# Optimization experiments

Measured on AMD Instinct MI355X. Metric: run time of the kernel, lower is better.

Reference implementation:

```python
import jax, jax.numpy as jnp
import numpy as np

N_NODES = 50000
N_EDGES = 400000


def setup_inputs() -> dict:
    key = jax.random.key(0)
    ks = jax.random.split(key, 8)
    d_in, d_hid, d_out = 512, 512, 256
    feats = jax.random.normal(ks[0], (N_NODES, d_in), dtype=jnp.float32)
    src = jax.random.randint(ks[1], (N_EDGES,), 0, N_NODES, dtype=jnp.int32)
    dst = jax.random.randint(ks[2], (N_EDGES,), 0, N_NODES, dtype=jnp.int32)
    # Glorot-ish scaled weights so activations stay O(1)
    W0 = jax.random.normal(ks[3], (d_in, d_hid), dtype=jnp.float32) / np.sqrt(d_in)
    b0 = jnp.zeros((d_hid,), jnp.float32)
    W1 = jax.random.normal(ks[4], (d_hid, d_hid), dtype=jnp.float32) / np.sqrt(d_hid)
    b1 = jnp.zeros((d_hid,), jnp.float32)
    W2 = jax.random.normal(ks[5], (d_hid, d_out), dtype=jnp.float32) / np.sqrt(d_hid)
    b2 = jnp.zeros((d_out,), jnp.float32)
    return {"feats": feats, "src": src, "dst": dst,
            "W0": W0, "b0": b0, "W1": W1, "b1": b1, "W2": W2, "b2": b2}


def _sage_conv_gcn(h, src, dst, W, b, deg):
    # DGL SAGEConv aggregator_type='gcn':
    # h_neigh[v] = (sum_{u->v} h[u] + h[v]) / (in_deg(v) + 1); out = h_neigh @ W + b
    agg = jax.ops.segment_sum(h[src], dst, num_segments=h.shape[0])  # [N, d]
    h_neigh = (agg + h) / (deg[:, None] + 1.0)
    return h_neigh @ W + b


def reference(feats, src, dst, W0, b0, W1, b1, W2, b2):
    N = feats.shape[0]
    deg = jax.ops.segment_sum(jnp.ones((src.shape[0],), feats.dtype), dst,
                              num_segments=N)  # in-degree per node
    h = jax.nn.relu(_sage_conv_gcn(feats, src, dst, W0, b0, deg))  # dropout p=0, norm none
    h = jax.nn.relu(_sage_conv_gcn(h, src, dst, W1, b1, deg))
    h = _sage_conv_gcn(h, src, dst, W2, b2, deg)  # final layer: no activation
    return h
```

## Files before the change

### kernel.cpp

```cpp
#include <hip/hip_runtime.h>
#include <stdint.h>

#define N_NODES 50000
#define N_EDGES 400000
#define MPAD    50048
#define SCAN_B  49

typedef __bf16 bf16x8 __attribute__((ext_vector_type(8)));
typedef float  f32x4  __attribute__((ext_vector_type(4)));
typedef unsigned short ushort_t;
typedef unsigned int   uint_t;

__device__ __forceinline__ ushort_t f2b(float f){
    uint_t x = __float_as_uint(f);
    x += 0x7FFFu + ((x >> 16) & 1u);
    return (ushort_t)(x >> 16);
}
__device__ __forceinline__ float b2f(ushort_t h){
    return __uint_as_float(((uint_t)h) << 16);
}

__device__ __forceinline__ int xcd_swz(int orig, int nwg){
    int q = nwg >> 3, r = nwg & 7;
    int xcd = orig & 7, idx = orig >> 3;
    int base = (xcd < r) ? xcd * (q + 1) : r * (q + 1) + (xcd - r) * q;
    return base + idx;
}

__global__ void zero_two(int* a, int* b, int n){
    int i = blockIdx.x * blockDim.x + threadIdx.x;
    if (i < n){ a[i] = 0; b[i] = 0; }
}

__global__ void hist_kernel(const int* __restrict__ dst, int* __restrict__ deg, int E){
    int i = blockIdx.x * blockDim.x + threadIdx.x;
    if (i < E) atomicAdd(&deg[dst[i]], 1);
}

__global__ __launch_bounds__(1024) void blk_scan_kernel(
        const int* __restrict__ deg, int* __restrict__ offs,
        int* __restrict__ bsum, int n){
    __shared__ int buf[1024];
    const int t = threadIdx.x, b = blockIdx.x;
    const int i = b * 1024 + t;
    int v = (i < n) ? deg[i] : 0;
    buf[t] = v; __syncthreads();
    for (int off = 1; off < 1024; off <<= 1){
        int x = (t >= off) ? buf[t - off] : 0;
        __syncthreads();
        buf[t] += x;
        __syncthreads();
    }
    if (i < n) offs[i] = buf[t] - v;
    if (t == 1023) bsum[b] = buf[1023];
}

__global__ void bsum_scan_kernel(int* __restrict__ bsum, int nb){
    int t = threadIdx.x;
    int orig = (t < nb) ? bsum[t] : 0;
    int v = orig;
    #pragma unroll
    for (int off = 1; off < 64; off <<= 1){
        int x = __shfl_up(v, off, 64);
        if (t >= off) v += x;
    }
    if (t < nb) bsum[t] = v - orig;
}

__global__ __launch_bounds__(1024) void add_off_kernel(
        int* __restrict__ offs, const int* __restrict__ bsum, int n){
    int i = blockIdx.x * 1024 + threadIdx.x;
    if (i < n) offs[i] += bsum[blockIdx.x];
    if (i == 0) offs[n] = N_EDGES;
}

__global__ void fill_kernel(const int* __restrict__ src, const int* __restrict__ dst,
                            const int* __restrict__ offs, int* __restrict__ cursor,
                            int* __restrict__ nbr, int E){
    int i = blockIdx.x * blockDim.x + threadIdx.x;
    if (i < E){
        int d = dst[i];
        int p = atomicAdd(&cursor[d], 1);
        nbr[offs[d] + p] = src[i];
    }
}

__global__ __launch_bounds__(256) void wtrans3_kernel(
        const float* __restrict__ W0, const float* __restrict__ W1,
        const float* __restrict__ W2, ushort_t* __restrict__ W0t,
        ushort_t* __restrict__ W1t, ushort_t* __restrict__ W2t){
    __shared__ float t[32][33];
    int b = blockIdx.x;
    const float* W; ushort_t* Wt; int K, N, bx, by;
    if (b < 256){            W = W0; Wt = W0t; K = 512; N = 512;
                             bx = (b & 15) * 32; by = (b >> 4) * 32; }
    else if (b < 512){ b -= 256; W = W1; Wt = W1t; K = 512; N = 512;
                             bx = (b & 15) * 32; by = (b >> 4) * 32; }
    else {             b -= 512; W = W2; Wt = W2t; K = 512; N = 256;
                             bx = (b & 7) * 32;  by = (b >> 3) * 32; }
    const int x = threadIdx.x & 31, y = threadIdx.x >> 5;
    #pragma unroll
    for (int j = 0; j < 32; j += 8)
        t[y + j][x] = W[(size_t)(by + y + j) * N + bx + x];
    __syncthreads();
    #pragma unroll
    for (int j = 0; j < 32; j += 8)
        Wt[(size_t)(bx + y + j) * K + by + x] = f2b(t[x][y + j]);
}

__device__ __forceinline__ void load16(const void* g, void* l){
    __builtin_amdgcn_global_load_lds((const __attribute__((address_space(1))) void*)g,
                                     (__attribute__((address_space(3))) void*)l, 16, 0, 0);
}

__global__ __launch_bounds__(256, 4) void gemm128_bt(const ushort_t* __restrict__ A,
                                                     const ushort_t* __restrict__ Bt,
                                                     ushort_t* __restrict__ C,
                                                     int NBN, int N, int K){
    __shared__ ushort_t As[128 * 64];
    __shared__ ushort_t Bs[128 * 64];
    const int tid  = threadIdx.x, lane = tid & 63, wave = tid >> 6;
    const int wg = xcd_swz(blockIdx.x, gridDim.x);
    const int bm = wg / NBN, bn = wg - bm * NBN;
    const int fr = lane & 15;
    const int wm = (wave >> 1) * 64, wn = (wave & 1) * 64;
    f32x4 acc[4][4] = {};

    for (int kt = 0; kt < K; kt += 64){
        __syncthreads();
        #pragma unroll
        for (int i = 0; i < 4; i++){
            int s = tid + i * 256;
            int row = s >> 3, p = s & 7, c = p ^ (row & 7);
            load16(A + (size_t)(bm * 128 + row) * K + kt + c * 8,
                   (char*)As + s * 16);
        }
        #pragma unroll
        for (int i = 0; i < 4; i++){
            int s = tid + i * 256;
            int row = s >> 3, p = s & 7, c = p ^ (row & 7);
            load16(Bt + (size_t)(bn * 128 + row) * K + kt + c * 8,
                   (char*)Bs + s * 16);
        }
        __syncthreads();
        #pragma unroll
        for (int ks = 0; ks < 2; ks++){
            const int c = (lane >> 4) + ks * 4;
            const int cx = c ^ (fr & 7);
            bf16x8 af[4], bf[4];
            #pragma unroll
            for (int t = 0; t < 4; t++)
                af[t] = *(const bf16x8*)(const void*)(As + (wm + t * 16 + fr) * 64 + cx * 8);
            #pragma unroll
            for (int t = 0; t < 4; t++)
                bf[t] = *(const bf16x8*)(const void*)(Bs + (wn + t * 16 + fr) * 64 + cx * 8);
            #pragma unroll
            for (int tm = 0; tm < 4; tm++)
                #pragma unroll
                for (int tn = 0; tn < 4; tn++)
                    acc[tm][tn] = __builtin_amdgcn_mfma_f32_16x16x32_bf16(
                                      af[tm], bf[tn], acc[tm][tn], 0, 0, 0);
        }
    }
    const int r0 = (lane >> 4) * 4, c0 = lane & 15;
    #pragma unroll
    for (int tm = 0; tm < 4; tm++){
        #pragma unroll
        for (int tn = 0; tn < 4; tn++){
            int rbase = bm * 128 + wm + tm * 16 + r0;
            int cidx  = bn * 128 + wn + tn * 16 + c0;
            #pragma unroll
            for (int reg = 0; reg < 4; reg++)
                C[(size_t)(rbase + reg) * N + cidx] = f2b(acc[tm][tn][reg]);
        }
    }
}

__global__ __launch_bounds__(256, 4) void gemm128_a32(const float* __restrict__ A,
                                                      const ushort_t* __restrict__ Bt,
                                                      ushort_t* __restrict__ C,
                                                      int K){
    __shared__ ushort_t As[128 * 64];
    __shared__ ushort_t Bs[128 * 64];
    const int tid  = threadIdx.x, lane = tid & 63, wave = tid >> 6;
    const int wg = xcd_swz(blockIdx.x, gridDim.x);
    const int bm = wg >> 2, bn = wg & 3;
    const int fr = lane & 15;
    const int wm = (wave >> 1) * 64, wn = (wave & 1) * 64;
    f32x4 acc[4][4] = {};

    for (int kt = 0; kt < K; kt += 64){
        __syncthreads();
        float4 x[4], y[4];
        #pragma unroll
        for (int i = 0; i < 4; i++){
            int s = tid + i * 256;
            int row = s >> 3, p = s & 7, c = p ^ (row & 7);
            int grow = bm * 128 + row;
            if (grow < N_NODES){
                const float* pp = A + (size_t)grow * K + kt + c * 8;
                x[i] = *(const float4*)(const void*)pp;
                y[i] = *(const float4*)(const void*)(pp + 4);
            } else {
                x[i] = make_float4(0.f, 0.f, 0.f, 0.f);
                y[i] = make_float4(0.f, 0.f, 0.f, 0.f);
            }
        }
        #pragma unroll
        for (int i = 0; i < 4; i++){
            int s = tid + i * 256;
            int row = s >> 3, p = s & 7, c = p ^ (row & 7);
            load16(Bt + (size_t)(bn * 128 + row) * K + kt + c * 8,
                   (char*)Bs + s * 16);
        }
        #pragma unroll
        for (int i = 0; i < 4; i++){
            int s = tid + i * 256;
            uint4 o;
            o.x = (uint_t)f2b(x[i].x) | ((uint_t)f2b(x[i].y) << 16);
            o.y = (uint_t)f2b(x[i].z) | ((uint_t)f2b(x[i].w) << 16);
            o.z = (uint_t)f2b(y[i].x) | ((uint_t)f2b(y[i].y) << 16);
            o.w = (uint_t)f2b(y[i].z) | ((uint_t)f2b(y[i].w) << 16);
            *(uint4*)(void*)((char*)As + s * 16) = o;
        }
        __syncthreads();
        #pragma unroll
        for (int ks = 0; ks < 2; ks++){
            const int c = (lane >> 4) + ks * 4;
            const int cx = c ^ (fr & 7);
            bf16x8 af[4], bf[4];
            #pragma unroll
            for (int t = 0; t < 4; t++)
                af[t] = *(const bf16x8*)(const void*)(As + (wm + t * 16 + fr) * 64 + cx * 8);
            #pragma unroll
            for (int t = 0; t < 4; t++)
                bf[t] = *(const bf16x8*)(const void*)(Bs + (wn + t * 16 + fr) * 64 + cx * 8);
            #pragma unroll
            for (int tm = 0; tm < 4; tm++)
                #pragma unroll
                for (int tn = 0; tn < 4; tn++)
                    acc[tm][tn] = __builtin_amdgcn_mfma_f32_16x16x32_bf16(
                                      af[tm], bf[tn], acc[tm][tn], 0, 0, 0);
        }
    }
    const int r0 = (lane >> 4) * 4, c0 = lane & 15;
    #pragma unroll
    for (int tm = 0; tm < 4; tm++){
        #pragma unroll
        for (int tn = 0; tn < 4; tn++){
            int rbase = bm * 128 + wm + tm * 16 + r0;
            int cidx  = bn * 128 + wn + tn * 16 + c0;
            #pragma unroll
            for (int reg = 0; reg < 4; reg++)
                C[(size_t)(rbase + reg) * 512 + cidx] = f2b(acc[tm][tn][reg]);
        }
    }
}

__device__ __forceinline__ void acc8(float* a, uint4 y){
    a[0] += b2f((ushort_t)(y.x & 0xffff)); a[1] += b2f((ushort_t)(y.x >> 16));
    a[2] += b2f((ushort_t)(y.y & 0xffff)); a[3] += b2f((ushort_t)(y.y >> 16));
    a[4] += b2f((ushort_t)(y.z & 0xffff)); a[5] += b2f((ushort_t)(y.z >> 16));
    a[6] += b2f((ushort_t)(y.w & 0xffff)); a[7] += b2f((ushort_t)(y.w >> 16));
}
__device__ __forceinline__ void acc4(float* a, uint2 y){
    a[0] += b2f((ushort_t)(y.x & 0xffff)); a[1] += b2f((ushort_t)(y.x >> 16));
    a[2] += b2f((ushort_t)(y.y & 0xffff)); a[3] += b2f((ushort_t)(y.y >> 16));
}

__global__ __launch_bounds__(256) void agg_relu_kernel(
        const ushort_t* __restrict__ Y, const int* __restrict__ offs,
        const int* __restrict__ nbr, const float* __restrict__ bias,
        ushort_t* __restrict__ H){
    const int lane = threadIdx.x & 63, wave = threadIdx.x >> 6;
    const int v0 = blockIdx.x * 8 + wave * 2, v1 = v0 + 1;
    const int off = lane * 8;
    float a0[8], a1[8];
    {   uint4 y = *(const uint4*)(const void*)(Y + (size_t)v0 * 512 + off);
        a0[0] = b2f((ushort_t)(y.x & 0xffff)); a0[1] = b2f((ushort_t)(y.x >> 16));
        a0[2] = b2f((ushort_t)(y.y & 0xffff)); a0[3] = b2f((ushort_t)(y.y >> 16));
        a0[4] = b2f((ushort_t)(y.z & 0xffff)); a0[5] = b2f((ushort_t)(y.z >> 16));
        a0[6] = b2f((ushort_t)(y.w & 0xffff)); a0[7] = b2f((ushort_t)(y.w >> 16)); }
    {   uint4 y = *(const uint4*)(const void*)(Y + (size_t)v1 * 512 + off);
        a1[0] = b2f((ushort_t)(y.x & 0xffff)); a1[1] = b2f((ushort_t)(y.x >> 16));
        a1[2] = b2f((ushort_t)(y.y & 0xffff)); a1[3] = b2f((ushort_t)(y.y >> 16));
        a1[4] = b2f((ushort_t)(y.z & 0xffff)); a1[5] = b2f((ushort_t)(y.z >> 16));
        a1[6] = b2f((ushort_t)(y.w & 0xffff)); a1[7] = b2f((ushort_t)(y.w >> 16)); }
    const int beg0 = offs[v0], end0 = offs[v0 + 1];
    const int beg1 = offs[v1], end1 = offs[v1 + 1];
    int i0 = beg0, i1 = beg1;
    while (i0 + 4 <= end0 && i1 + 4 <= end1){
        uint4 yy0[4], yy1[4];
        #pragma unroll
        for (int j = 0; j < 4; j++){
            int u = nbr[i0 + j];
            yy0[j] = *(const uint4*)(const void*)(Y + (size_t)u * 512 + off);
        }
        #pragma unroll
        for (int j = 0; j < 4; j++){
            int u = nbr[i1 + j];
            yy1[j] = *(const uint4*)(const void*)(Y + (size_t)u * 512 + off);
        }
        #pragma unroll
        for (int j = 0; j < 4; j++) acc8(a0, yy0[j]);
        #pragma unroll
        for (int j = 0; j < 4; j++) acc8(a1, yy1[j]);
        i0 += 4; i1 += 4;
    }
    for (; i0 + 4 <= end0; i0 += 4){
        uint4 yy[4];
        #pragma unroll
        for (int j = 0; j < 4; j++){
            int u = nbr[i0 + j];
            yy[j] = *(const uint4*)(const void*)(Y + (size_t)u * 512 + off);
        }
        #pragma unroll
        for (int j = 0; j < 4; j++) acc8(a0, yy[j]);
    }
    for (; i0 < end0; i0++){
        int u = nbr[i0];
        uint4 y = *(const uint4*)(const void*)(Y + (size_t)u * 512 + off);
        acc8(a0, y);
    }
    for (; i1 + 4 <= end1; i1 += 4){
        uint4 yy[4];
        #pragma unroll
        for (int j = 0; j < 4; j++){
            int u = nbr[i1 + j];
            yy[j] = *(const uint4*)(const void*)(Y + (size_t)u * 512 + off);
        }
        #pragma unroll
        for (int j = 0; j < 4; j++) acc8(a1, yy[j]);
    }
    for (; i1 < end1; i1++){
        int u = nbr[i1];
        uint4 y = *(const uint4*)(const void*)(Y + (size_t)u * 512 + off);
        acc8(a1, y);
    }
    float4 bb0 = ((const float4*)bias)[lane * 2];
    float4 bb1 = ((const float4*)bias)[lane * 2 + 1];
    {
        const float inv = 1.0f / (float)(end0 - beg0 + 1);
        float r[8];
        r[0] = a0[0]*inv + bb0.x; r[1] = a0[1]*inv + bb0.y;
        r[2] = a0[2]*inv + bb0.z; r[3] = a0[3]*inv + bb0.w;
        r[4] = a0[4]*inv + bb1.x; r[5] = a0[5]*inv + bb1.y;
        r[6] = a0[6]*inv + bb1.z; r[7] = a0[7]*inv + bb1.w;
        #pragma unroll
        for (int j = 0; j < 8; j++) r[j] = r[j] > 0.f ? r[j] : 0.f;
        uint4 o;
        o.x = (uint_t)f2b(r[0]) | ((uint_t)f2b(r[1]) << 16);
        o.y = (uint_t)f2b(r[2]) | ((uint_t)f2b(r[3]) << 16);
        o.z = (uint_t)f2b(r[4]) | ((uint_t)f2b(r[5]) << 16);
        o.w = (uint_t)f2b(r[6]) | ((uint_t)f2b(r[7]) << 16);
        *(uint4*)(void*)(H + (size_t)v0 * 512 + off) = o;
    }
    {
        const float inv = 1.0f / (float)(end1 - beg1 + 1);
        float r[8];
        r[0] = a1[0]*inv + bb0.x; r[1] = a1[1]*inv + bb0.y;
        r[2] = a1[2]*inv + bb0.z; r[3] = a1[3]*inv + bb0.w;
        r[4] = a1[4]*inv + bb1.x; r[5] = a1[5]*inv + bb1.y;
        r[6] = a1[6]*inv + bb1.z; r[7] = a1[7]*inv + bb1.w;
        #pragma unroll
        for (int j = 0; j < 8; j++) r[j] = r[j] > 0.f ? r[j] : 0.f;
        uint4 o;
        o.x = (uint_t)f2b(r[0]) | ((uint_t)f2b(r[1]) << 16);
        o.y = (uint_t)f2b(r[2]) | ((uint_t)f2b(r[3]) << 16);
        o.z = (uint_t)f2b(r[4]) | ((uint_t)f2b(r[5]) << 16);
        o.w = (uint_t)f2b(r[6]) | ((uint_t)f2b(r[7]) << 16);
        *(uint4*)(void*)(H + (size_t)v1 * 512 + off) = o;
    }
}

__global__ __launch_bounds__(256) void agg_out_kernel(
        const ushort_t* __restrict__ Y, const int* __restrict__ offs,
        const int* __restrict__ nbr, const float* __restrict__ bias,
        float* __restrict__ out){
    const int lane = threadIdx.x & 63, wave = threadIdx.x >> 6;
    const int v = blockIdx.x * 4 + wave;
    const int off = lane * 4;
    float a[4];
    {   uint2 y = *(const uint2*)(const void*)(Y + (size_t)v * 256 + off);
        a[0] = b2f((ushort_t)(y.x & 0xffff)); a[1] = b2f((ushort_t)(y.x >> 16));
        a[2] = b2f((ushort_t)(y.y & 0xffff)); a[3] = b2f((ushort_t)(y.y >> 16)); }
    const int beg = offs[v], end = offs[v + 1];
    int i = beg;
    for (; i + 8 <= end; i += 8){
        uint2 yy[8];
        #pragma unroll
        for (int j = 0; j < 8; j++){
            int u = nbr[i + j];
            yy[j] = *(const uint2*)(const void*)(Y + (size_t)u * 256 + off);
        }
        #pragma unroll
        for (int j = 0; j < 8; j++) acc4(a, yy[j]);
    }
    for (; i + 4 <= end; i += 4){
        uint2 yy[4];
        #pragma unroll
        for (int j = 0; j < 4; j++){
            int u = nbr[i + j];
            yy[j] = *(const uint2*)(const void*)(Y + (size_t)u * 256 + off);
        }
        #pragma unroll
        for (int j = 0; j < 4; j++) acc4(a, yy[j]);
    }
    for (; i < end; i++){
        int u = nbr[i];
        uint2 y = *(const uint2*)(const void*)(Y + (size_t)u * 256 + off);
        acc4(a, y);
    }
    const float inv = 1.0f / (float)(end - beg + 1);
    float4 bb = ((const float4*)bias)[lane];
    float4 r;
    r.x = a[0]*inv + bb.x; r.y = a[1]*inv + bb.y;
    r.z = a[2]*inv + bb.z; r.w = a[3]*inv + bb.w;
    ((float4*)out)[v * 64 + lane] = r;
}

extern "C" void kernel_launch(void* const* d_in, const int* in_sizes, int n_in,
                              void* d_out, int out_size, void* d_ws, size_t ws_size,
                              hipStream_t stream) {
    const float* feats = (const float*)d_in[0];
    const int*   src   = (const int*)  d_in[1];
    const int*   dst   = (const int*)  d_in[2];
    const float* W0    = (const float*)d_in[3];
    const float* b0    = (const float*)d_in[4];
    const float* W1    = (const float*)d_in[5];
    const float* b1    = (const float*)d_in[6];
    const float* W2    = (const float*)d_in[7];
    const float* b2    = (const float*)d_in[8];
    float* out = (float*)d_out;

    char* w = (char*)d_ws;
    ushort_t* Abuf = (ushort_t*)w;  w += (size_t)MPAD * 512 * 2;
    ushort_t* Ybuf = (ushort_t*)w;  w += (size_t)MPAD * 512 * 2;
    ushort_t* W0t  = (ushort_t*)w;  w += 512 * 512 * 2;
    ushort_t* W1t  = (ushort_t*)w;  w += 512 * 512 * 2;
    ushort_t* W2t  = (ushort_t*)w;  w += 256 * 512 * 2;
    int* deg    = (int*)w;          w += 50048 * 4;
    int* offs   = (int*)w;          w += 50056 * 4;
    int* cursor = (int*)w;          w += 50048 * 4;
    int* nbr    = (int*)w;          w += (size_t)N_EDGES * 4;
    int* bsum   = (int*)w;          w += 64 * 4;

    zero_two<<<(N_NODES + 255) / 256, 256, 0, stream>>>(deg, cursor, N_NODES);
    hist_kernel<<<(N_EDGES + 255) / 256, 256, 0, stream>>>(dst, deg, N_EDGES);
    blk_scan_kernel<<<SCAN_B, 1024, 0, stream>>>(deg, offs, bsum, N_NODES);
    bsum_scan_kernel<<<1, 64, 0, stream>>>(bsum, SCAN_B);
    add_off_kernel<<<SCAN_B, 1024, 0, stream>>>(offs, bsum, N_NODES);
    fill_kernel<<<(N_EDGES + 255) / 256, 256, 0, stream>>>(src, dst, offs, cursor, nbr, N_EDGES);

    wtrans3_kernel<<<640, 256, 0, stream>>>(W0, W1, W2, W0t, W1t, W2t);

    const int g01 = (MPAD / 128) * 4;
    const int g2  = (MPAD / 128) * 2;

    gemm128_a32<<<g01, 256, 0, stream>>>(feats, W0t, Ybuf, 512);
    agg_relu_kernel<<<N_NODES / 8, 256, 0, stream>>>(Ybuf, offs, nbr, b0, Abuf);
    gemm128_bt<<<g01, 256, 0, stream>>>(Abuf, W1t, Ybuf, 4, 512, 512);
    agg_relu_kernel<<<N_NODES / 8, 256, 0, stream>>>(Ybuf, offs, nbr, b1, Abuf);
    gemm128_bt<<<g2, 256, 0, stream>>>(Abuf, W2t, Ybuf, 2, 256, 512);
    agg_out_kernel<<<N_NODES / 4, 256, 0, stream>>>(Ybuf, offs, nbr, b2, out);
}
```

Before: 478.4 us.

## Fuse CSR preprocessing into weight-transpose and first GEMM launches

Merges the zeroing of the degree and cursor arrays into the weight-transpose kernel. It also appends the degree-histogram atomics as extra blocks of the first GEMM grid, so they overlap with GEMM work, and replaces the three-kernel scan with a single-block scan. Together these cut the preprocessing from seven launches to four, reducing launch gaps and idle tails. The single-block scan serialises 49 elements per thread with strided, uncoalesced reads, and histogram blocks now compete with GEMM blocks for CUs.

```diff
diff --git a/kernel.cpp b/kernel.cpp
--- a/kernel.cpp
+++ b/kernel.cpp
@@ -4,7 +4,8 @@
 #define N_NODES 50000
 #define N_EDGES 400000
 #define MPAD    50048
-#define SCAN_B  49
+#define G_GEMM  1564
+#define H_BLKS  1563
 
 typedef __bf16 bf16x8 __attribute__((ext_vector_type(8)));
 typedef float  f32x4  __attribute__((ext_vector_type(4)));
@@ -27,51 +28,64 @@
     return base + idx;
 }
 
-__global__ void zero_two(int* a, int* b, int n){
-    int i = blockIdx.x * blockDim.x + threadIdx.x;
-    if (i < n){ a[i] = 0; b[i] = 0; }
-}
-
-__global__ void hist_kernel(const int* __restrict__ dst, int* __restrict__ deg, int E){
-    int i = blockIdx.x * blockDim.x + threadIdx.x;
-    if (i < E) atomicAdd(&deg[dst[i]], 1);
-}
-
-__global__ __launch_bounds__(1024) void blk_scan_kernel(
-        const int* __restrict__ deg, int* __restrict__ offs,
-        int* __restrict__ bsum, int n){
-    __shared__ int buf[1024];
-    const int t = threadIdx.x, b = blockIdx.x;
-    const int i = b * 1024 + t;
-    int v = (i < n) ? deg[i] : 0;
-    buf[t] = v; __syncthreads();
+__global__ __launch_bounds__(256) void pre_kernel(
+        const float* __restrict__ W0, const float* __restrict__ W1,
+        const float* __restrict__ W2, ushort_t* __restrict__ W0t,
+        ushort_t* __restrict__ W1t, ushort_t* __restrict__ W2t,
+        int* __restrict__ deg, int* __restrict__ cursor){
+    int b = blockIdx.x;
+    if (b >= 640){
+        int i = (b - 640) * 256 + threadIdx.x;
+        if (i < N_NODES){ deg[i] = 0; cursor[i] = 0; }
+        return;
+    }
+    __shared__ float t[32][33];
+    const float* W; ushort_t* Wt; int K, N, bx, by;
+    if (b < 256){            W = W0; Wt = W0t; K = 512; N = 512;
+                             bx = (b & 15) * 32; by = (b >> 4) * 32; }
+    else if (b < 512){ b -= 256; W = W1; Wt = W1t; K = 512; N = 512;
+                             bx = (b & 15) * 32; by = (b >> 4) * 32; }
+    else {             b -= 512; W = W2; Wt = W2t; K = 512; N = 256;
+                             bx = (b & 7) * 32;  by = (b >> 3) * 32; }
+    const int x = threadIdx.x & 31, y = threadIdx.x >> 5;
+    #pragma unroll
+    for (int j = 0; j < 32; j += 8)
+        t[y + j][x] = W[(size_t)(by + y + j) * N + bx + x];
+    __syncthreads();
+    #pragma unroll
+    for (int j = 0; j < 32; j += 8)
+        Wt[(size_t)(bx + y + j) * K + by + x] = f2b(t[x][y + j]);
+}
+
+__global__ __launch_bounds__(1024) void scan50k(const int* __restrict__ deg,
+                                                int* __restrict__ offs){
+    __shared__ int sums[1024];
+    const int t = threadIdx.x;
+    const int base = t * 49;
+    int s = 0;
+    #pragma unroll
+    for (int j = 0; j < 49; j++){
+        int i = base + j;
+        s += (i < N_NODES) ? deg[i] : 0;
+    }
+    sums[t] = s; __syncthreads();
     for (int off = 1; off < 1024; off <<= 1){
-        int x = (t >= off) ? buf[t - off] : 0;
-        __syncthreads();
-        buf[t] += x;
-        __syncthreads();
-    }
-    if (i < n) offs[i] = buf[t] - v;
-    if (t == 1023) bsum[b] = buf[1023];
-}
-
-__global__ void bsum_scan_kernel(int* __restrict__ bsum, int nb){
-    int t = threadIdx.x;
-    int orig = (t < nb) ? bsum[t] : 0;
-    int v = orig;
-    #pragma unroll
-    for (int off = 1; off < 64; off <<= 1){
-        int x = __shfl_up(v, off, 64);
-        if (t >= off) v += x;
-    }
-    if (t < nb) bsum[t] = v - orig;
-}
-
-__global__ __launch_bounds__(1024) void add_off_kernel(
-        int* __restrict__ offs, const int* __restrict__ bsum, int n){
-    int i = blockIdx.x * 1024 + threadIdx.x;
-    if (i < n) offs[i] += bsum[blockIdx.x];
-    if (i == 0) offs[n] = N_EDGES;
+        int x = (t >= off) ? sums[t - off] : 0;
+        __syncthreads();
+        sums[t] += x;
+        __syncthreads();
+    }
+    int excl = sums[t] - s;
+    #pragma unroll
+    for (int j = 0; j < 49; j++){
+        int i = base + j;
+        if (i < N_NODES){
+            int v = deg[i];
+            offs[i] = excl;
+            excl += v;
+        }
+    }
+    if (t == 0) offs[N_NODES] = N_EDGES;
 }
 
 __global__ void fill_kernel(const int* __restrict__ src, const int* __restrict__ dst,
@@ -83,29 +97,6 @@
         int p = atomicAdd(&cursor[d], 1);
         nbr[offs[d] + p] = src[i];
     }
-}
-
-__global__ __launch_bounds__(256) void wtrans3_kernel(
-        const float* __restrict__ W0, const float* __restrict__ W1,
-        const float* __restrict__ W2, ushort_t* __restrict__ W0t,
-        ushort_t* __restrict__ W1t, ushort_t* __restrict__ W2t){
-    __shared__ float t[32][33];
-    int b = blockIdx.x;
-    const float* W; ushort_t* Wt; int K, N, bx, by;
-    if (b < 256){            W = W0; Wt = W0t; K = 512; N = 512;
-                             bx = (b & 15) * 32; by = (b >> 4) * 32; }
-    else if (b < 512){ b -= 256; W = W1; Wt = W1t; K = 512; N = 512;
-                             bx = (b & 15) * 32; by = (b >> 4) * 32; }
-    else {             b -= 512; W = W2; Wt = W2t; K = 512; N = 256;
-                             bx = (b & 7) * 32;  by = (b >> 3) * 32; }
-    const int x = threadIdx.x & 31, y = threadIdx.x >> 5;
-    #pragma unroll
-    for (int j = 0; j < 32; j += 8)
-        t[y + j][x] = W[(size_t)(by + y + j) * N + bx + x];
-    __syncthreads();
-    #pragma unroll
-    for (int j = 0; j < 32; j += 8)
-        Wt[(size_t)(bx + y + j) * K + by + x] = f2b(t[x][y + j]);
 }
 
 __device__ __forceinline__ void load16(const void* g, void* l){
@@ -176,14 +167,21 @@
     }
 }
 
-__global__ __launch_bounds__(256, 4) void gemm128_a32(const float* __restrict__ A,
-                                                      const ushort_t* __restrict__ Bt,
-                                                      ushort_t* __restrict__ C,
-                                                      int K){
+__global__ __launch_bounds__(256, 4) void gemm128_a32h(const float* __restrict__ A,
+                                                       const ushort_t* __restrict__ Bt,
+                                                       ushort_t* __restrict__ C,
+                                                       const int* __restrict__ dst,
+                                                       int* __restrict__ deg,
+                                                       int K){
     __shared__ ushort_t As[128 * 64];
     __shared__ ushort_t Bs[128 * 64];
+    if (blockIdx.x >= G_GEMM){
+        int i = (blockIdx.x - G_GEMM) * 256 + threadIdx.x;
+        if (i < N_EDGES) atomicAdd(&deg[dst[i]], 1);
+        return;
+    }
     const int tid  = threadIdx.x, lane = tid & 63, wave = tid >> 6;
-    const int wg = xcd_swz(blockIdx.x, gridDim.x);
+    const int wg = xcd_swz(blockIdx.x, G_GEMM);
     const int bm = wg >> 2, bn = wg & 3;
     const int fr = lane & 15;
     const int wm = (wave >> 1) * 64, wn = (wave & 1) * 64;
@@ -445,22 +443,13 @@
     int* nbr    = (int*)w;          w += (size_t)N_EDGES * 4;
     int* bsum   = (int*)w;          w += 64 * 4;
 
-    zero_two<<<(N_NODES + 255) / 256, 256, 0, stream>>>(deg, cursor, N_NODES);
-    hist_kernel<<<(N_EDGES + 255) / 256, 256, 0, stream>>>(dst, deg, N_EDGES);
-    blk_scan_kernel<<<SCAN_B, 1024, 0, stream>>>(deg, offs, bsum, N_NODES);
-    bsum_scan_kernel<<<1, 64, 0, stream>>>(bsum, SCAN_B);
-    add_off_kernel<<<SCAN_B, 1024, 0, stream>>>(offs, bsum, N_NODES);
-    fill_kernel<<<(N_EDGES + 255) / 256, 256, 0, stream>>>(src, dst, offs, cursor, nbr, N_EDGES);
-
-    wtrans3_kernel<<<640, 256, 0, stream>>>(W0, W1, W2, W0t, W1t, W2t);
-
-    const int g01 = (MPAD / 128) * 4;
-    const int g2  = (MPAD / 128) * 2;
-
-    gemm128_a32<<<g01, 256, 0, stream>>>(feats, W0t, Ybuf, 512);
+    pre_kernel<<<836, 256, 0, stream>>>(W0, W1, W2, W0t, W1t, W2t, deg, cursor);
+    gemm128_a32h<<<G_GEMM + H_BLKS, 256, 0, stream>>>(feats, W0t, Ybuf, dst, deg, 512);
+    scan50k<<<1, 1024, 0, stream>>>(deg, offs);
+    fill_kernel<<<H_BLKS, 256, 0, stream>>>(src, dst, offs, cursor, nbr, N_EDGES);
     agg_relu_kernel<<<N_NODES / 8, 256, 0, stream>>>(Ybuf, offs, nbr, b0, Abuf);
-    gemm128_bt<<<g01, 256, 0, stream>>>(Abuf, W1t, Ybuf, 4, 512, 512);
+    gemm128_bt<<<(MPAD / 128) * 4, 256, 0, stream>>>(Abuf, W1t, Ybuf, 4, 512, 512);
     agg_relu_kernel<<<N_NODES / 8, 256, 0, stream>>>(Ybuf, offs, nbr, b1, Abuf);
-    gemm128_bt<<<g2, 256, 0, stream>>>(Abuf, W2t, Ybuf, 2, 256, 512);
+    gemm128_bt<<<(MPAD / 128) * 2, 256, 0, stream>>>(Abuf, W2t, Ybuf, 2, 256, 512);
     agg_out_kernel<<<N_NODES / 4, 256, 0, stream>>>(Ybuf, offs, nbr, b2, out);
 }
```

Result: slower. 547.3 us (+14.4%).
